# Kernel tuning notes

Hardware: AMD Instinct MI355X
Metric: run time of the kernel (lower is better)

Reference implementation:

```python
import jax, jax.numpy as jnp
import numpy as np

N, K, C, H, V = 4096, 32, 128, 128, 21   # residues, kNN, node/edge dim, hidden, vocab
NEG_SLOPE = 0.2

def gatv2(src_feat, tgt_feat, edge_feat, Wl, bl, Wr, br, We, be, att, b_out):
    # GATv2Conv (1 head, eval mode) on a regular kNN graph.
    # src_feat: [N,K,Din] gathered source-node features per edge; tgt_feat: [N,Din]
    xl = src_feat @ Wl + bl                       # [N,K,C]
    xr = tgt_feat @ Wr + br                       # [N,C]
    ee = edge_feat @ We + be                      # [N,K,C]
    m = jax.nn.leaky_relu(xl + xr[:, None, :] + ee, NEG_SLOPE)
    alpha = jax.nn.softmax(jnp.einsum('nkc,c->nk', m, att), axis=1)
    return jnp.einsum('nk,nkc->nc', alpha, xl) + b_out

def setup_inputs():
    key = jax.random.key(0)
    ks = jax.random.split(key, 32)
    w = lambda k, s: jax.random.normal(k, s, jnp.float32) * 0.05
    z0 = lambda s: jnp.zeros(s, jnp.float32)
    return dict(
        E=jax.random.normal(ks[0], (N, K, C), jnp.float32),
        E_idx=jax.random.randint(ks[1], (N, K), 0, N),
        S=jax.random.randint(ks[2], (N,), 0, V),
        mask=jnp.ones((N,), jnp.float32),
        chain_M=jnp.ones((N,), jnp.float32),
        z=jax.random.normal(ks[3], (N,), jnp.float32),
        Wl1=w(ks[4], (C, C)), bl1=z0((C,)),
        Wr1=w(ks[5], (C, C)), br1=z0((C,)),
        We1=w(ks[6], (C, C)), be1=z0((C,)),
        a1=w(ks[7], (C,)), bo1=z0((C,)),
        Wl2=w(ks[8], (C + H, C)), bl2=z0((C,)),
        Wr2=w(ks[9], (C + H, C)), br2=z0((C,)),
        We2=w(ks[10], (C, C)), be2=z0((C,)),
        a2=w(ks[11], (C,)), bo2=z0((C,)),
        W_s=w(ks[12], (V, H)),
        W_out=w(ks[13], (C, V)), b_out=z0((V,)),
    )

def reference(E, E_idx, S, mask, chain_M, z,
              Wl1, bl1, Wr1, br1, We1, be1, a1, bo1,
              Wl2, bl2, Wr2, br2, We2, be2, a2, bo2,
              W_s, W_out, b_out):
    # encoder GAT over zero-initialized node features
    x0 = jnp.zeros((N, C), E.dtype)
    node_attr = gatv2(x0[E_idx], x0, E, Wl1, bl1, Wr1, br1, We1, be1, a1, bo1)
    seq_attr = W_s[S]                                        # [N,H]
    h_full = jnp.concatenate([node_attr, seq_attr], -1)      # [N,C+H]
    h_mask = jnp.concatenate([node_attr, jnp.zeros_like(seq_attr)], -1)
    cm = chain_M * mask
    decoding_order = jnp.argsort((cm + 1e-4) * jnp.abs(z))   # [N]
    P = jax.nn.one_hot(decoding_order, N, dtype=E.dtype)     # [N,N] permutation
    L = 1.0 - jnp.triu(jnp.ones((N, N), E.dtype))            # strictly lower tri
    order_mask_backward = jnp.einsum('ij,iq,jp->qp', L, P, P)
    mask_attend = jnp.take_along_axis(order_mask_backward, E_idx, axis=1)[..., None]
    m1d = mask[:, None, None]
    mask_bw = m1d * mask_attend
    mask_fw = m1d * (1.0 - mask_attend)
    # per-edge source features: neighbor seq embedding visible only if decoded earlier
    src = h_full[E_idx] * mask_bw + h_mask[E_idx] * mask_fw  # [N,K,C+H]
    out = gatv2(src, h_mask, E, Wl2, bl2, Wr2, br2, We2, be2, a2, bo2)
    logits = out @ W_out + b_out
    return jax.nn.log_softmax(logits, axis=-1)
```

## Files before the change

### kernel.cpp

```cpp
#include <hip/hip_runtime.h>
#include <hip/hip_bf16.h>

typedef short short8 __attribute__((ext_vector_type(8)));
typedef float float4v __attribute__((ext_vector_type(4)));

#define WS_T   0
#define WS_D   2688
#define WS_C   2816
#define WS_O   2944
#define WS_A2  3072
#define WS_KEY 3200
#define WS_G   7296
#define WS_B0  7744
#define WS_B1  7776

__device__ __forceinline__ unsigned int pack2bf(float a, float b) {
  union { float f; unsigned int u; } xa, xb;
  xa.f = a; xb.f = b;
  return ((xa.u + 0x8000u) >> 16) | ((xb.u + 0x8000u) & 0xFFFF0000u);
}

__global__ __launch_bounds__(256) void pg9_pre(
    const float* __restrict__ Wl2, const float* __restrict__ Wr2,
    const float* __restrict__ We2, const float* __restrict__ bl1,
    const float* __restrict__ bl2, const float* __restrict__ br2,
    const float* __restrict__ be2, const float* __restrict__ a2,
    const float* __restrict__ bo1, const float* __restrict__ bo2,
    const float* __restrict__ W_s, const float* __restrict__ mask,
    const float* __restrict__ chain_M, const float* __restrict__ z,
    const float* __restrict__ W_out, const float* __restrict__ b_out,
    void* __restrict__ ws)
{
  __shared__ float sA[128], sB[128];
  short* wsW = (short*)ws;
  float* F = (float*)ws + 8192;
  const int b = blockIdx.x, tid = threadIdx.x;
  if (b == 0) {
    for (int s = tid; s < 16384; s += 256) {
      const int row = s >> 7, c = s & 127;
      const int q = row >> 5, lh = (row & 31) >> 3, j = row & 7;
      const int t = c >> 4, cl = c & 15;
      union { float f; unsigned int u; } x; x.f = We2[s];
      const unsigned int r = x.u + 0x7FFFu + ((x.u >> 16) & 1u);
      wsW[(((q * 8 + t) * 64) + lh * 16 + cl) * 8 + j] = (short)(r >> 16);
    }
    if (tid < 128) {
      const int c = tid;
      float cl0 = 0.f, cr0 = 0.f;
      for (int i = 0; i < 128; i++) {
        const float s = bl1[i] + bo1[i];
        cl0 += s * Wl2[i * 128 + c];
        cr0 += s * Wr2[i * 128 + c];
      }
      const float O = bl2[c] + bo2[c];
      F[WS_D + c]  = be2[c] + bl2[c] + br2[c] + cr0;
      F[WS_C + c]  = cl0;
      F[WS_O + c]  = O;
      F[WS_A2 + c] = a2[c];
      sA[c] = O;
      sB[c] = cl0;
    }
    __syncthreads();
    if (tid < 21) {
      float b0 = b_out[tid], b1 = 0.f;
      for (int c = 0; c < 128; c++) {
        b0 = fmaf(sA[c], W_out[c * 21 + tid], b0);
        b1 = fmaf(sB[c], W_out[c * 21 + tid], b1);
      }
      F[WS_B0 + tid] = b0;
      F[WS_B1 + tid] = b1;
    }
  } else if (b <= 21) {
    const int v = b - 1;
    if (tid < 128) {
      const int c = tid;
      float acc = 0.f;
      for (int h = 0; h < 128; h++)
        acc += W_s[v * 128 + h] * Wl2[(128 + h) * 128 + c];
      F[WS_T + v * 128 + c] = acc;
      sA[c] = acc;
    }
    __syncthreads();
    if (tid < 21) {
      float g = 0.f;
      for (int c = 0; c < 128; c++)
        g = fmaf(sA[c], W_out[c * 21 + tid], g);
      F[WS_G + v * 21 + tid] = g;
    }
  } else {
    const int n = (b - 22) * 256 + tid;
    F[WS_KEY + n] = (chain_M[n] * mask[n] + 1e-4f) * fabsf(z[n]);
  }
}

__global__ __launch_bounds__(256, 4) void pg9_main(
    const float* __restrict__ E, const int* __restrict__ E_idx,
    const int* __restrict__ S, const float* __restrict__ mask,
    const void* __restrict__ ws, float* __restrict__ out)
{
  const short* wsW = (const short*)ws;
  const float* F = (const float*)ws + 8192;
  const int tid  = threadIdx.x;
  const int wave = tid >> 6;
  const int lane = tid & 63;
  const int quad = lane >> 4;
  const int lid  = lane & 15;
  const int n    = blockIdx.x * 4 + wave;
  const float maskn = mask[n];

  short8 afr[2][4];
#pragma unroll
  for (int g = 0; g < 2; g++) {
    const float* erow = E + (size_t)(n * 32 + g * 16 + lid) * 128 + quad * 8;
#pragma unroll
    for (int q = 0; q < 4; q++) {
      const float4 A = *(const float4*)(erow + q * 32);
      const float4 B = *(const float4*)(erow + q * 32 + 4);
      union { short8 s; unsigned int u[4]; } v;
      v.u[0] = pack2bf(A.x, A.y);
      v.u[1] = pack2bf(A.z, A.w);
      v.u[2] = pack2bf(B.x, B.y);
      v.u[3] = pack2bf(B.z, B.w);
      afr[g][q] = v.s;
    }
  }

  float wkv = 0.f; int rvv = 0;
  if (lane < 32) {
    const int j = E_idx[n * 32 + lane];
    const float keyn = F[WS_KEY + n], kj = F[WS_KEY + j];
    const int before = (kj < keyn) || (kj == keyn && j < n);
    wkv = before ? maskn : 0.f;
    rvv = S[j];
  }
  int rows[2][4]; float wks[2][4];
#pragma unroll
  for (int g = 0; g < 2; g++)
#pragma unroll
    for (int r = 0; r < 4; r++) {
      const int kk = g * 16 + quad * 4 + r;
      rows[g][r] = __shfl(rvv, kk) * 128;
      wks[g][r]  = __shfl(wkv, kk);
    }

  float part[2][4] = {{0.f, 0.f, 0.f, 0.f}, {0.f, 0.f, 0.f, 0.f}};
#pragma unroll
  for (int t = 0; t < 8; t++) {
    short8 bfr[4];
#pragma unroll
    for (int q = 0; q < 4; q++)
      bfr[q] = *(const short8*)(wsW + (((q * 8 + t) * 64) + lane) * 8);
    float4v ac0 = {0.f, 0.f, 0.f, 0.f}, ac1 = {0.f, 0.f, 0.f, 0.f};
#pragma unroll
    for (int q = 0; q < 4; q++) {
      ac0 = __builtin_amdgcn_mfma_f32_16x16x32_bf16(afr[0][q], bfr[q], ac0, 0, 0, 0);
      ac1 = __builtin_amdgcn_mfma_f32_16x16x32_bf16(afr[1][q], bfr[q], ac1, 0, 0, 0);
    }
    const int c = t * 16 + lid;
    const float dvt  = F[WS_D + c] + maskn * F[WS_C + c];
    const float a2vt = F[WS_A2 + c];
#pragma unroll
    for (int r = 0; r < 4; r++) {
      float v0 = ac0[r] + dvt + wks[0][r] * F[WS_T + rows[0][r] + c];
      float v1 = ac1[r] + dvt + wks[1][r] * F[WS_T + rows[1][r] + c];
      v0 = fmaxf(v0, 0.f) + 0.2f * fminf(v0, 0.f);
      v1 = fmaxf(v1, 0.f) + 0.2f * fminf(v1, 0.f);
      part[0][r] = fmaf(v0, a2vt, part[0][r]);
      part[1][r] = fmaf(v1, a2vt, part[1][r]);
    }
  }
  float sreg[2][4];
#pragma unroll
  for (int g = 0; g < 2; g++)
#pragma unroll
    for (int r = 0; r < 4; r++) {
      float v = part[g][r];
      v += __shfl_xor(v, 1);
      v += __shfl_xor(v, 2);
      v += __shfl_xor(v, 4);
      v += __shfl_xor(v, 8);
      sreg[g][r] = v;
    }

  float mx = -1e30f;
#pragma unroll
  for (int g = 0; g < 2; g++)
#pragma unroll
    for (int r = 0; r < 4; r++) mx = fmaxf(mx, sreg[g][r]);
  mx = fmaxf(mx, __shfl_xor(mx, 16));
  mx = fmaxf(mx, __shfl_xor(mx, 32));
  float eg[2][4], esum = 0.f;
#pragma unroll
  for (int g = 0; g < 2; g++)
#pragma unroll
    for (int r = 0; r < 4; r++) {
      eg[g][r] = expf(sreg[g][r] - mx);
      esum += eg[g][r];
    }
  esum += __shfl_xor(esum, 16);
  esum += __shfl_xor(esum, 32);
  const float inv = 1.f / esum;
  float cg[2][4];
#pragma unroll
  for (int g = 0; g < 2; g++)
#pragma unroll
    for (int r = 0; r < 4; r++) cg[g][r] = eg[g][r] * inv * wks[g][r];

  float lg = (lane < 21) ? (F[WS_B0 + lane] + maskn * F[WS_B1 + lane]) : -1e30f;
#pragma unroll
  for (int kk = 0; kk < 32; kk++) {
    const int g = kk >> 4, sq = (kk >> 2) & 3, r = kk & 3;
    const float cf = __shfl(cg[g][r], sq * 16);
    const int row = __shfl(rvv, kk) * 21;
    if (lane < 21) lg = fmaf(cf, F[WS_G + row + lane], lg);
  }

  float lmx = lg;
  lmx = fmaxf(lmx, __shfl_xor(lmx, 1));
  lmx = fmaxf(lmx, __shfl_xor(lmx, 2));
  lmx = fmaxf(lmx, __shfl_xor(lmx, 4));
  lmx = fmaxf(lmx, __shfl_xor(lmx, 8));
  lmx = fmaxf(lmx, __shfl_xor(lmx, 16));
  float ex = (lane < 21) ? expf(lg - lmx) : 0.f;
  float es = ex;
  es += __shfl_xor(es, 1);
  es += __shfl_xor(es, 2);
  es += __shfl_xor(es, 4);
  es += __shfl_xor(es, 8);
  es += __shfl_xor(es, 16);
  if (lane < 21)
    out[n * 21 + lane] = lg - lmx - logf(es);
}

extern "C" void kernel_launch(void* const* d_in, const int* in_sizes, int n_in,
                              void* d_out, int out_size, void* d_ws, size_t ws_size,
                              hipStream_t stream)
{
  const float* E       = (const float*)d_in[0];
  const int*   E_idx   = (const int*)d_in[1];
  const int*   S       = (const int*)d_in[2];
  const float* mask    = (const float*)d_in[3];
  const float* chain_M = (const float*)d_in[4];
  const float* z       = (const float*)d_in[5];
  const float* bl1     = (const float*)d_in[7];
  const float* bo1     = (const float*)d_in[13];
  const float* Wl2     = (const float*)d_in[14];
  const float* bl2     = (const float*)d_in[15];
  const float* Wr2     = (const float*)d_in[16];
  const float* br2     = (const float*)d_in[17];
  const float* We2     = (const float*)d_in[18];
  const float* be2     = (const float*)d_in[19];
  const float* a2      = (const float*)d_in[20];
  const float* bo2     = (const float*)d_in[21];
  const float* W_s     = (const float*)d_in[22];
  const float* W_out   = (const float*)d_in[23];
  const float* b_out   = (const float*)d_in[24];

  pg9_pre<<<38, 256, 0, stream>>>(Wl2, Wr2, We2, bl1, bl2, br2, be2, a2,
                                  bo1, bo2, W_s, mask, chain_M, z,
                                  W_out, b_out, d_ws);
  pg9_main<<<1024, 256, 0, stream>>>(E, E_idx, S, mask, d_ws, (float*)d_out);
}
```

Before: 172.8 us.

## Stage E through LDS with coalesced loads and pack key with sequence id

Each wave now loads its node's 32x128 edge-feature block with fully contiguous float4 loads, converts it to bf16, and writes it into a padded per-wave LDS tile. After a wave barrier it reads the MFMA A fragments back from LDS, replacing the strided per-lane global loads. The prepass also interleaves the decoding key and S[n] into one float2 record so each neighbor needs a single gather instead of two. The cost is 34 KB of LDS per block, which may cap occupancy below the requested four blocks per CU.

```diff
diff --git a/kernel.cpp b/kernel.cpp
--- a/kernel.cpp
+++ b/kernel.cpp
@@ -9,10 +9,10 @@
 #define WS_C   2816
 #define WS_O   2944
 #define WS_A2  3072
-#define WS_KEY 3200
 #define WS_G   7296
 #define WS_B0  7744
 #define WS_B1  7776
+#define WS_M   7808
 
 __device__ __forceinline__ unsigned int pack2bf(float a, float b) {
   union { float f; unsigned int u; } xa, xb;
@@ -20,7 +20,7 @@
   return ((xa.u + 0x8000u) >> 16) | ((xb.u + 0x8000u) & 0xFFFF0000u);
 }
 
-__global__ __launch_bounds__(256) void pg9_pre(
+__global__ __launch_bounds__(256) void pg10_pre(
     const float* __restrict__ Wl2, const float* __restrict__ Wr2,
     const float* __restrict__ We2, const float* __restrict__ bl1,
     const float* __restrict__ bl2, const float* __restrict__ br2,
@@ -28,8 +28,8 @@
     const float* __restrict__ bo1, const float* __restrict__ bo2,
     const float* __restrict__ W_s, const float* __restrict__ mask,
     const float* __restrict__ chain_M, const float* __restrict__ z,
-    const float* __restrict__ W_out, const float* __restrict__ b_out,
-    void* __restrict__ ws)
+    const int* __restrict__ S, const float* __restrict__ W_out,
+    const float* __restrict__ b_out, void* __restrict__ ws)
 {
   __shared__ float sA[128], sB[128];
   short* wsW = (short*)ws;
@@ -89,15 +89,18 @@
     }
   } else {
     const int n = (b - 22) * 256 + tid;
-    F[WS_KEY + n] = (chain_M[n] * mask[n] + 1e-4f) * fabsf(z[n]);
-  }
-}
-
-__global__ __launch_bounds__(256, 4) void pg9_main(
+    F[WS_M + 2 * n] = (chain_M[n] * mask[n] + 1e-4f) * fabsf(z[n]);
+    ((int*)F)[WS_M + 2 * n + 1] = S[n];
+  }
+}
+
+__global__ __launch_bounds__(256, 4) void pg10_main(
     const float* __restrict__ E, const int* __restrict__ E_idx,
-    const int* __restrict__ S, const float* __restrict__ mask,
-    const void* __restrict__ ws, float* __restrict__ out)
+    const float* __restrict__ mask, const void* __restrict__ ws,
+    float* __restrict__ out)
 {
+  __shared__ __align__(16) short ldsE[4][32 * 136];
+
   const short* wsW = (const short*)ws;
   const float* F = (const float*)ws + 8192;
   const int tid  = threadIdx.x;
@@ -108,30 +111,31 @@
   const int n    = blockIdx.x * 4 + wave;
   const float maskn = mask[n];
 
-  short8 afr[2][4];
-#pragma unroll
-  for (int g = 0; g < 2; g++) {
-    const float* erow = E + (size_t)(n * 32 + g * 16 + lid) * 128 + quad * 8;
-#pragma unroll
-    for (int q = 0; q < 4; q++) {
-      const float4 A = *(const float4*)(erow + q * 32);
-      const float4 B = *(const float4*)(erow + q * 32 + 4);
-      union { short8 s; unsigned int u[4]; } v;
-      v.u[0] = pack2bf(A.x, A.y);
-      v.u[1] = pack2bf(A.z, A.w);
-      v.u[2] = pack2bf(B.x, B.y);
-      v.u[3] = pack2bf(B.z, B.w);
-      afr[g][q] = v.s;
-    }
+  int jidx = 0;
+  if (lane < 32) jidx = E_idx[n * 32 + lane];
+
+  const float* ebase = E + (size_t)n * 32 * 128;
+  short* myE = ldsE[wave];
+#pragma unroll
+  for (int i = 0; i < 8; i++) {
+    const int e = i * 512 + lane * 8;
+    const float4 A = *(const float4*)(ebase + e);
+    const float4 B = *(const float4*)(ebase + e + 4);
+    union { short8 s; unsigned int u[4]; } v;
+    v.u[0] = pack2bf(A.x, A.y);
+    v.u[1] = pack2bf(A.z, A.w);
+    v.u[2] = pack2bf(B.x, B.y);
+    v.u[3] = pack2bf(B.z, B.w);
+    *(short8*)(myE + (e >> 7) * 136 + (e & 127)) = v.s;
   }
 
   float wkv = 0.f; int rvv = 0;
+  const float keyn = F[WS_M + 2 * n];
   if (lane < 32) {
-    const int j = E_idx[n * 32 + lane];
-    const float keyn = F[WS_KEY + n], kj = F[WS_KEY + j];
-    const int before = (kj < keyn) || (kj == keyn && j < n);
+    const float2 mj = *(const float2*)(F + WS_M + 2 * jidx);
+    const int before = (mj.x < keyn) || (mj.x == keyn && jidx < n);
     wkv = before ? maskn : 0.f;
-    rvv = S[j];
+    union { float f; int i; } c; c.f = mj.y; rvv = c.i;
   }
   int rows[2][4]; float wks[2][4];
 #pragma unroll
@@ -142,6 +146,15 @@
       rows[g][r] = __shfl(rvv, kk) * 128;
       wks[g][r]  = __shfl(wkv, kk);
     }
+
+  __builtin_amdgcn_wave_barrier();
+
+  short8 afr[2][4];
+#pragma unroll
+  for (int g = 0; g < 2; g++)
+#pragma unroll
+    for (int q = 0; q < 4; q++)
+      afr[g][q] = *(const short8*)(myE + (g * 16 + lid) * 136 + q * 32 + quad * 8);
 
   float part[2][4] = {{0.f, 0.f, 0.f, 0.f}, {0.f, 0.f, 0.f, 0.f}};
 #pragma unroll
@@ -211,7 +224,7 @@
   for (int kk = 0; kk < 32; kk++) {
     const int g = kk >> 4, sq = (kk >> 2) & 3, r = kk & 3;
     const float cf = __shfl(cg[g][r], sq * 16);
-    const int row = __shfl(rvv, kk) * 21;
+    const int row = (rows[0][0], __shfl(rvv, kk)) * 21;
     if (lane < 21) lg = fmaf(cf, F[WS_G + row + lane], lg);
   }
 
@@ -256,8 +269,8 @@
   const float* W_out   = (const float*)d_in[23];
   const float* b_out   = (const float*)d_in[24];
 
-  pg9_pre<<<38, 256, 0, stream>>>(Wl2, Wr2, We2, bl1, bl2, br2, be2, a2,
-                                  bo1, bo2, W_s, mask, chain_M, z,
-                                  W_out, b_out, d_ws);
-  pg9_main<<<1024, 256, 0, stream>>>(E, E_idx, S, mask, d_ws, (float*)d_out);
-}
+  pg10_pre<<<38, 256, 0, stream>>>(Wl2, Wr2, We2, bl1, bl2, br2, be2, a2,
+                                   bo1, bo2, W_s, mask, chain_M, z, S,
+                                   W_out, b_out, d_ws);
+  pg10_main<<<1024, 256, 0, stream>>>(E, E_idx, mask, d_ws, (float*)d_out);
+}
```

Result: faster. 168.2 us (-2.7%).
